# Performance work log

Measured on AMD Instinct MI355X. Metric: run time of the kernel, lower is better.

## Reference

```python
import jax, jax.numpy as jnp
import numpy as np

NUM_EMBEDDINGS = 8192
EMBEDDING_DIM = 32
L2_EPS = 1e-12  # matches torch F.normalize eps


def _l2_normalize(x, axis=-1):
    norm = jnp.linalg.norm(x, axis=axis, keepdims=True)
    return x / jnp.maximum(norm, L2_EPS)


def setup_inputs() -> dict:
    key = jax.random.key(0)
    k1, k2 = jax.random.split(key)
    inputs = jax.random.normal(k1, (32, 1024, EMBEDDING_DIM), dtype=jnp.float32)
    embeddings = jax.random.normal(k2, (NUM_EMBEDDINGS, EMBEDDING_DIM), dtype=jnp.float32)
    embeddings = _l2_normalize(embeddings, axis=1)  # buffer init: F.normalize(randn)
    return {"inputs": inputs, "embeddings": embeddings}


def reference(inputs, embeddings):
    input_shape = inputs.shape
    d = embeddings.shape[1]
    flat = inputs.reshape(-1, d)                      # [N, d]
    flat_n = _l2_normalize(flat, axis=1)              # F.normalize(flat, p=2, dim=1)
    # cosine similarity against codebook: [N, K]
    distances = jnp.einsum('nd,kd->nk', flat_n, embeddings)
    encoding_indices = jnp.argmax(distances, axis=1)  # [N]
    quantized = embeddings[encoding_indices].reshape(input_shape)
    # use_commitment=False branch: mse(quantized, inputs.detach())
    loss = jnp.mean((quantized - jax.lax.stop_gradient(inputs)) ** 2)
    # straight-through estimator
    quantized_st = inputs + jax.lax.stop_gradient(quantized - inputs)
    return quantized_st, loss, encoding_indices.reshape(input_shape[:-1])
```

## Files before the change

### kernel.cpp

```cpp
#include <hip/hip_runtime.h>

typedef short short8 __attribute__((ext_vector_type(8)));
typedef float f32x4 __attribute__((ext_vector_type(4)));

#define NROWS 32768
#define DIM 32
#define KCODES 8192
#define FLAG_CAP 16384
#define EPS_REL (1.0f/4096.0f)

#define WS_EHI  0
#define WS_ELO  (512*1024)
#define WS_PART (1024*1024)
#define WS_CNT  (WS_PART + 4096)
#define WS_LIST (WS_CNT + 64)
#define WS_CORR (WS_LIST + FLAG_CAP*4)

__device__ __forceinline__ unsigned short bf16_rne(float v){
    unsigned int u = __float_as_uint(v);
    unsigned int r = (u + 0x7fffu + ((u >> 16) & 1u)) >> 16;
    return (unsigned short)r;
}
__device__ __forceinline__ float bf16_to_f(unsigned short h){
    return __uint_as_float(((unsigned int)h) << 16);
}
__device__ __forceinline__ float dot4(const float4& a, const float4& b){
    return fmaf(a.w, b.w, fmaf(a.z, b.z, fmaf(a.y, b.y, a.x * b.x)));
}

__global__ __launch_bounds__(256) void vq_prep(
    const float* __restrict__ emb,
    unsigned short* __restrict__ ehi, unsigned short* __restrict__ elo,
    int* __restrict__ cnt)
{
    int r = blockIdx.x * 256 + threadIdx.x;
    if (r == 0) cnt[0] = 0;
    const float* er = emb + (size_t)r * DIM;
    short8* dh = (short8*)(ehi + (size_t)r * DIM);
    short8* dl = (short8*)(elo + (size_t)r * DIM);
    #pragma unroll
    for (int i = 0; i < 4; i++){
        float4 v0 = *(const float4*)(er + i*8);
        float4 v1 = *(const float4*)(er + i*8 + 4);
        float f[8] = {v0.x, v0.y, v0.z, v0.w, v1.x, v1.y, v1.z, v1.w};
        short8 a, b;
        #pragma unroll
        for (int j = 0; j < 8; j++){
            unsigned short h = bf16_rne(f[j]);
            a[j] = (short)h;
            b[j] = (short)bf16_rne(f[j] - bf16_to_f(h));
        }
        dh[i] = a; dl[i] = b;
    }
}

#define PROC(bhv, blv, tcs)                                                      \
  {                                                                              \
    unsigned int tcv = (unsigned int)(tcs);                                      \
    _Pragma("unroll")                                                            \
    for (int rg = 0; rg < 4; ++rg){                                              \
      f32x4 acc = __builtin_amdgcn_mfma_f32_16x16x32_bf16(ahi[rg], bhv, cbias[rg], 0, 0, 0); \
      acc = __builtin_amdgcn_mfma_f32_16x16x32_bf16(ahi[rg], blv, acc, 0, 0, 0); \
      acc = __builtin_amdgcn_mfma_f32_16x16x32_bf16(alo[rg], bhv, acc, 0, 0, 0); \
      _Pragma("unroll")                                                          \
      for (int q = 0; q < 4; ++q){                                               \
        unsigned int u = (__float_as_uint(acc[q]) & maskv) | tcv;                \
        int rr = rg * 4 + q;                                                     \
        unsigned int nv2;                                                        \
        asm("v_med3_u32 %0, %1, %2, %3" : "=v"(nv2) : "v"(u), "v"(v1[rr]), "v"(v2[rr])); \
        v2[rr] = nv2;                                                            \
        v1[rr] = max(u, v1[rr]);                                                 \
      }                                                                          \
    }                                                                            \
  }

__global__ __launch_bounds__(512, 4) void vq_main_mfma(
    const float* __restrict__ inputs,
    const unsigned short* __restrict__ ehi,
    const unsigned short* __restrict__ elo,
    const float* __restrict__ emb,
    float* __restrict__ out_q, float* __restrict__ out_idx,
    float* __restrict__ part, int* __restrict__ cnt, int* __restrict__ list)
{
    const int L = threadIdx.x & 63;
    const int w = threadIdx.x >> 6;
    const int rowbase = blockIdx.x * 64;

    __shared__ float snorm[64];
    __shared__ unsigned int sv1[8][64];
    __shared__ unsigned int sv2[8][64];
    __shared__ int          scol[8][64];

    short8 ahi[4], alo[4];
    #pragma unroll
    for (int rg = 0; rg < 4; ++rg){
        const float* xr = inputs + (size_t)(rowbase + rg*16 + (L & 15)) * DIM + (L >> 4) * 8;
        float4 p0 = *(const float4*)xr;
        float4 p1 = *(const float4*)(xr + 4);
        float f[8] = {p0.x, p0.y, p0.z, p0.w, p1.x, p1.y, p1.z, p1.w};
        short8 h, l;
        #pragma unroll
        for (int i = 0; i < 8; i++){
            unsigned short hb = bf16_rne(f[i]);
            h[i] = (short)hb;
            l[i] = (short)bf16_rne(f[i] - bf16_to_f(hb));
        }
        ahi[rg] = h; alo[rg] = l;
        float s = dot4(p0, p0) + dot4(p1, p1);
        s += __shfl_xor(s, 16, 64);
        s += __shfl_xor(s, 32, 64);
        if (w == 0 && (L >> 4) == 0) snorm[rg*16 + L] = sqrtf(s);
    }
    __syncthreads();

    f32x4 cbias[4];
    #pragma unroll
    for (int rg = 0; rg < 4; ++rg){
        #pragma unroll
        for (int q = 0; q < 4; ++q)
            cbias[rg][q] = 2.0f * snorm[rg*16 + (L >> 4)*4 + q];
    }

    unsigned int maskv = 0xFFFFFFC0u;
    asm("" : "+v"(maskv));

    unsigned int v1[16], v2[16];
    #pragma unroll
    for (int r = 0; r < 16; r++){ v1[r] = 0u; v2[r] = 0u; }

    const int c0 = w * 1024;
    const unsigned short* ehp = ehi + (size_t)(c0 + (L & 15)) * DIM + (L >> 4) * 8;
    const unsigned short* elp = elo + (size_t)(c0 + (L & 15)) * DIM + (L >> 4) * 8;

    for (int t = 0; t < 64; t += 2){
        short8 b0h = *(const short8*)(ehp);
        short8 b0l = *(const short8*)(elp);
        short8 b1h = *(const short8*)(ehp + 512);
        short8 b1l = *(const short8*)(elp + 512);
        ehp += 1024; elp += 1024;
        PROC(b0h, b0l, 63 - t);
        PROC(b1h, b1l, 62 - t);
    }

    unsigned int p1[16];
    #pragma unroll
    for (int r = 0; r < 16; r++) p1[r] = v1[r];
    #pragma unroll
    for (int m = 1; m < 16; m <<= 1){
        #pragma unroll
        for (int r = 0; r < 16; r++){
            unsigned int ov1 = __shfl_xor(v1[r], m, 64);
            unsigned int ov2 = __shfl_xor(v2[r], m, 64);
            unsigned int mn = min(v1[r], ov1);
            v2[r] = max(max(v2[r], ov2), mn);
            v1[r] = max(v1[r], ov1);
        }
    }
    int colr[16];
    #pragma unroll
    for (int r = 0; r < 16; r++){
        unsigned long long bm = __ballot(p1[r] == v1[r]);
        unsigned int grp = (unsigned int)((bm >> ((L >> 4) << 4)) & 0xFFFFull);
        colr[r] = __ffs(grp) - 1;
    }

    if ((L & 15) == 0){
        #pragma unroll
        for (int rg = 0; rg < 4; ++rg){
            #pragma unroll
            for (int q = 0; q < 4; ++q){
                int row = rg*16 + (L >> 4)*4 + q;
                sv1[w][row] = v1[rg*4 + q];
                sv2[w][row] = v2[rg*4 + q];
                scol[w][row] = colr[rg*4 + q];
            }
        }
    }
    __syncthreads();

    if (threadIdx.x < 64){
        int r = threadIdx.x;
        unsigned int b1 = 0u, b2 = 0u; int bw = 0, bc = 0;
        #pragma unroll
        for (int s = 0; s < 8; ++s){
            unsigned int u1 = sv1[s][r];
            unsigned int u2 = sv2[s][r];
            unsigned int mn = min(b1, u1);
            b2 = max(max(b2, u2), mn);
            bool g = u1 > b1;
            if (g){ b1 = u1; bw = s; bc = scol[s][r]; }
        }
        int t = 63 - (int)(b1 & 63u);
        int k = bw*1024 + t*16 + bc;
        int row = rowbase + r;
        out_idx[row] = (float)k;

        const float4* ep = (const float4*)(emb + (size_t)k * DIM);
        const float4* xr = (const float4*)(inputs + (size_t)row * DIM);
        float4* oq = (float4*)(out_q + (size_t)row * DIM);
        float s = 0.f;
        #pragma unroll
        for (int i = 0; i < 8; i++){
            float4 q = ep[i], x = xr[i];
            oq[i] = q;
            float dx = q.x - x.x, dy = q.y - x.y, dz = q.z - x.z, dw = q.w - x.w;
            s += dx*dx + dy*dy + dz*dz + dw*dw;
        }

        float f1 = __uint_as_float(b1 & 0xFFFFFFC0u);
        float f2 = __uint_as_float(b2 & 0xFFFFFFC0u);
        if (f1 - f2 <= snorm[r] * EPS_REL){
            int pos = atomicAdd(cnt, 1);
            if (pos < FLAG_CAP) list[pos] = row;
        }

        #pragma unroll
        for (int off = 32; off; off >>= 1) s += __shfl_down(s, off, 64);
        if (r == 0) part[blockIdx.x] = s;
    }
}

__global__ __launch_bounds__(256) void vq_refine(
    const float* __restrict__ inputs, const float* __restrict__ emb,
    float* __restrict__ out_q, float* __restrict__ out_idx,
    const int* __restrict__ list, const int* __restrict__ cnt,
    float* __restrict__ corrd)
{
    int n = *cnt; if (n > FLAG_CAP) n = FLAG_CAP;
    __shared__ float sv[4]; __shared__ int si[4];
    __shared__ int sbi;
    for (int j = blockIdx.x; j < n; j += gridDim.x){
        int row = list[j];
        const float4* xr = (const float4*)(inputs + (size_t)row * DIM);
        float4 x0 = xr[0], x1 = xr[1], x2 = xr[2], x3 = xr[3];
        float4 x4 = xr[4], x5 = xr[5], x6 = xr[6], x7 = xr[7];
        float bv = -3.0e38f; int bi = 0x7fffffff;
        for (int c = threadIdx.x; c < KCODES; c += 256){
            const float4* ep = (const float4*)(emb + (size_t)c * DIM);
            float d = dot4(x0, ep[0]) + dot4(x1, ep[1]) + dot4(x2, ep[2]) + dot4(x3, ep[3])
                    + dot4(x4, ep[4]) + dot4(x5, ep[5]) + dot4(x6, ep[6]) + dot4(x7, ep[7]);
            if (d > bv || (d == bv && c < bi)){ bv = d; bi = c; }
        }
        #pragma unroll
        for (int off = 32; off; off >>= 1){
            float ov = __shfl_down(bv, off, 64);
            int   oi = __shfl_down(bi, off, 64);
            if (ov > bv || (ov == bv && oi < bi)){ bv = ov; bi = oi; }
        }
        if ((threadIdx.x & 63) == 0){ sv[threadIdx.x >> 6] = bv; si[threadIdx.x >> 6] = bi; }
        __syncthreads();
        if (threadIdx.x == 0){
            #pragma unroll
            for (int q = 1; q < 4; q++){
                if (sv[q] > bv || (sv[q] == bv && si[q] < bi)){ bv = sv[q]; bi = si[q]; }
            }
            sbi = bi;
        }
        __syncthreads();
        int knew = sbi;
        int kold = (int)out_idx[row];
        if (threadIdx.x < 32){
            float x  = inputs[(size_t)row * DIM + threadIdx.x];
            float en = emb[(size_t)knew * DIM + threadIdx.x];
            float eo = emb[(size_t)kold * DIM + threadIdx.x];
            float d  = (en - x)*(en - x) - (eo - x)*(eo - x);
            #pragma unroll
            for (int off = 16; off; off >>= 1) d += __shfl_down(d, off, 64);
            if (knew != kold) out_q[(size_t)row * DIM + threadIdx.x] = en;
            if (threadIdx.x == 0){
                corrd[j] = (knew != kold) ? d : 0.0f;
                if (knew != kold) out_idx[row] = (float)knew;
            }
        }
        __syncthreads();
    }
}

__global__ __launch_bounds__(256) void vq_loss(
    const float* __restrict__ part, const float* __restrict__ corrd,
    const int* __restrict__ cnt, float* __restrict__ out_loss)
{
    int n = *cnt; if (n > FLAG_CAP) n = FLAG_CAP;
    float s = 0.f;
    for (int i = threadIdx.x; i < 512; i += 256) s += part[i];
    for (int j = threadIdx.x; j < n; j += 256) s += corrd[j];
    #pragma unroll
    for (int off = 32; off; off >>= 1) s += __shfl_down(s, off, 64);
    __shared__ float sp[4];
    if ((threadIdx.x & 63) == 0) sp[threadIdx.x >> 6] = s;
    __syncthreads();
    if (threadIdx.x == 0)
        *out_loss = (sp[0] + sp[1] + sp[2] + sp[3]) * (1.0f / ((float)NROWS * (float)DIM));
}

extern "C" void kernel_launch(void* const* d_in, const int* in_sizes, int n_in,
                              void* d_out, int out_size, void* d_ws, size_t ws_size,
                              hipStream_t stream) {
    const float* inputs = (const float*)d_in[0];
    const float* emb    = (const float*)d_in[1];
    float* out      = (float*)d_out;
    float* out_q    = out;
    float* out_loss = out + (size_t)NROWS * DIM;
    float* out_idx  = out_loss + 1;

    char* ws = (char*)d_ws;
    unsigned short* ehi   = (unsigned short*)(ws + WS_EHI);
    unsigned short* elo   = (unsigned short*)(ws + WS_ELO);
    float*          part  = (float*)(ws + WS_PART);
    int*            cnt   = (int*)(ws + WS_CNT);
    int*            list  = (int*)(ws + WS_LIST);
    float*          corrd = (float*)(ws + WS_CORR);

    vq_prep     <<<dim3(KCODES/256), dim3(256), 0, stream>>>(emb, ehi, elo, cnt);
    vq_main_mfma<<<dim3(NROWS/64),   dim3(512), 0, stream>>>(inputs, ehi, elo, emb,
                                                             out_q, out_idx, part, cnt, list);
    vq_refine   <<<dim3(256),        dim3(256), 0, stream>>>(inputs, emb, out_q, out_idx,
                                                             list, cnt, corrd);
    vq_loss     <<<dim3(1),          dim3(256), 0, stream>>>(part, corrd, cnt, out_loss);
}
```

Baseline: 98.76 us.

## Halve rows per block, fuse loss into refine, widen prep parallelism

The main MFMA kernel now handles 32 rows per block instead of 64, giving 1024 blocks instead of 512, with launch bounds raised to 8 waves per SIMD. The aim is to spread work over more CUs and raise occupancy. The separate loss kernel is removed: the last refine block to finish, detected with an atomic ticket counter, sums the partials. The prep kernel splits each codebook row across 4 threads. The trade-off is that each codebook tile loaded from memory is reused across half as many rows, so codebook traffic per row doubles.

```diff
diff --git a/kernel.cpp b/kernel.cpp
--- a/kernel.cpp
+++ b/kernel.cpp
@@ -8,6 +8,7 @@
 #define KCODES 8192
 #define FLAG_CAP 16384
 #define EPS_REL (1.0f/4096.0f)
+#define NBLK 1024
 
 #define WS_EHI  0
 #define WS_ELO  (512*1024)
@@ -33,32 +34,30 @@
     unsigned short* __restrict__ ehi, unsigned short* __restrict__ elo,
     int* __restrict__ cnt)
 {
-    int r = blockIdx.x * 256 + threadIdx.x;
-    if (r == 0) cnt[0] = 0;
-    const float* er = emb + (size_t)r * DIM;
-    short8* dh = (short8*)(ehi + (size_t)r * DIM);
-    short8* dl = (short8*)(elo + (size_t)r * DIM);
-    #pragma unroll
-    for (int i = 0; i < 4; i++){
-        float4 v0 = *(const float4*)(er + i*8);
-        float4 v1 = *(const float4*)(er + i*8 + 4);
-        float f[8] = {v0.x, v0.y, v0.z, v0.w, v1.x, v1.y, v1.z, v1.w};
-        short8 a, b;
-        #pragma unroll
-        for (int j = 0; j < 8; j++){
-            unsigned short h = bf16_rne(f[j]);
-            a[j] = (short)h;
-            b[j] = (short)bf16_rne(f[j] - bf16_to_f(h));
-        }
-        dh[i] = a; dl[i] = b;
-    }
+    int tid = blockIdx.x * 256 + threadIdx.x;
+    if (tid < 2) cnt[tid] = 0;
+    int r  = tid >> 2;
+    int qt = tid & 3;
+    const float* er = emb + (size_t)r * DIM + qt * 8;
+    float4 v0 = *(const float4*)er;
+    float4 v1 = *(const float4*)(er + 4);
+    float f[8] = {v0.x, v0.y, v0.z, v0.w, v1.x, v1.y, v1.z, v1.w};
+    short8 a, b;
+    #pragma unroll
+    for (int j = 0; j < 8; j++){
+        unsigned short h = bf16_rne(f[j]);
+        a[j] = (short)h;
+        b[j] = (short)bf16_rne(f[j] - bf16_to_f(h));
+    }
+    *(short8*)(ehi + (size_t)r * DIM + qt * 8) = a;
+    *(short8*)(elo + (size_t)r * DIM + qt * 8) = b;
 }
 
 #define PROC(bhv, blv, tcs)                                                      \
   {                                                                              \
     unsigned int tcv = (unsigned int)(tcs);                                      \
     _Pragma("unroll")                                                            \
-    for (int rg = 0; rg < 4; ++rg){                                              \
+    for (int rg = 0; rg < 2; ++rg){                                              \
       f32x4 acc = __builtin_amdgcn_mfma_f32_16x16x32_bf16(ahi[rg], bhv, cbias[rg], 0, 0, 0); \
       acc = __builtin_amdgcn_mfma_f32_16x16x32_bf16(ahi[rg], blv, acc, 0, 0, 0); \
       acc = __builtin_amdgcn_mfma_f32_16x16x32_bf16(alo[rg], bhv, acc, 0, 0, 0); \
@@ -74,7 +73,7 @@
     }                                                                            \
   }
 
-__global__ __launch_bounds__(512, 4) void vq_main_mfma(
+__global__ __launch_bounds__(512, 8) void vq_main_mfma(
     const float* __restrict__ inputs,
     const unsigned short* __restrict__ ehi,
     const unsigned short* __restrict__ elo,
@@ -84,16 +83,16 @@
 {
     const int L = threadIdx.x & 63;
     const int w = threadIdx.x >> 6;
-    const int rowbase = blockIdx.x * 64;
-
-    __shared__ float snorm[64];
-    __shared__ unsigned int sv1[8][64];
-    __shared__ unsigned int sv2[8][64];
-    __shared__ int          scol[8][64];
-
-    short8 ahi[4], alo[4];
-    #pragma unroll
-    for (int rg = 0; rg < 4; ++rg){
+    const int rowbase = blockIdx.x * 32;
+
+    __shared__ float snorm[32];
+    __shared__ unsigned int sv1[8][32];
+    __shared__ unsigned int sv2[8][32];
+    __shared__ int          scol[8][32];
+
+    short8 ahi[2], alo[2];
+    #pragma unroll
+    for (int rg = 0; rg < 2; ++rg){
         const float* xr = inputs + (size_t)(rowbase + rg*16 + (L & 15)) * DIM + (L >> 4) * 8;
         float4 p0 = *(const float4*)xr;
         float4 p1 = *(const float4*)(xr + 4);
@@ -113,9 +112,9 @@
     }
     __syncthreads();
 
-    f32x4 cbias[4];
-    #pragma unroll
-    for (int rg = 0; rg < 4; ++rg){
+    f32x4 cbias[2];
+    #pragma unroll
+    for (int rg = 0; rg < 2; ++rg){
         #pragma unroll
         for (int q = 0; q < 4; ++q)
             cbias[rg][q] = 2.0f * snorm[rg*16 + (L >> 4)*4 + q];
@@ -124,9 +123,9 @@
     unsigned int maskv = 0xFFFFFFC0u;
     asm("" : "+v"(maskv));
 
-    unsigned int v1[16], v2[16];
-    #pragma unroll
-    for (int r = 0; r < 16; r++){ v1[r] = 0u; v2[r] = 0u; }
+    unsigned int v1[8], v2[8];
+    #pragma unroll
+    for (int r = 0; r < 8; r++){ v1[r] = 0u; v2[r] = 0u; }
 
     const int c0 = w * 1024;
     const unsigned short* ehp = ehi + (size_t)(c0 + (L & 15)) * DIM + (L >> 4) * 8;
@@ -142,13 +141,13 @@
         PROC(b1h, b1l, 62 - t);
     }
 
-    unsigned int p1[16];
-    #pragma unroll
-    for (int r = 0; r < 16; r++) p1[r] = v1[r];
+    unsigned int p1[8];
+    #pragma unroll
+    for (int r = 0; r < 8; r++) p1[r] = v1[r];
     #pragma unroll
     for (int m = 1; m < 16; m <<= 1){
         #pragma unroll
-        for (int r = 0; r < 16; r++){
+        for (int r = 0; r < 8; r++){
             unsigned int ov1 = __shfl_xor(v1[r], m, 64);
             unsigned int ov2 = __shfl_xor(v2[r], m, 64);
             unsigned int mn = min(v1[r], ov1);
@@ -156,9 +155,9 @@
             v1[r] = max(v1[r], ov1);
         }
     }
-    int colr[16];
-    #pragma unroll
-    for (int r = 0; r < 16; r++){
+    int colr[8];
+    #pragma unroll
+    for (int r = 0; r < 8; r++){
         unsigned long long bm = __ballot(p1[r] == v1[r]);
         unsigned int grp = (unsigned int)((bm >> ((L >> 4) << 4)) & 0xFFFFull);
         colr[r] = __ffs(grp) - 1;
@@ -166,7 +165,7 @@
 
     if ((L & 15) == 0){
         #pragma unroll
-        for (int rg = 0; rg < 4; ++rg){
+        for (int rg = 0; rg < 2; ++rg){
             #pragma unroll
             for (int q = 0; q < 4; ++q){
                 int row = rg*16 + (L >> 4)*4 + q;
@@ -178,7 +177,7 @@
     }
     __syncthreads();
 
-    if (threadIdx.x < 64){
+    if (threadIdx.x < 32){
         int r = threadIdx.x;
         unsigned int b1 = 0u, b2 = 0u; int bw = 0, bc = 0;
         #pragma unroll
@@ -215,7 +214,7 @@
         }
 
         #pragma unroll
-        for (int off = 32; off; off >>= 1) s += __shfl_down(s, off, 64);
+        for (int off = 16; off; off >>= 1) s += __shfl_down(s, off, 64);
         if (r == 0) part[blockIdx.x] = s;
     }
 }
@@ -223,10 +222,11 @@
 __global__ __launch_bounds__(256) void vq_refine(
     const float* __restrict__ inputs, const float* __restrict__ emb,
     float* __restrict__ out_q, float* __restrict__ out_idx,
-    const int* __restrict__ list, const int* __restrict__ cnt,
-    float* __restrict__ corrd)
+    const int* __restrict__ list, int* __restrict__ cnt,
+    float* __restrict__ corrd, const float* __restrict__ part,
+    float* __restrict__ out_loss)
 {
-    int n = *cnt; if (n > FLAG_CAP) n = FLAG_CAP;
+    int n = cnt[0]; if (n > FLAG_CAP) n = FLAG_CAP;
     __shared__ float sv[4]; __shared__ int si[4];
     __shared__ int sbi;
     for (int j = blockIdx.x; j < n; j += gridDim.x){
@@ -274,23 +274,26 @@
         }
         __syncthreads();
     }
-}
-
-__global__ __launch_bounds__(256) void vq_loss(
-    const float* __restrict__ part, const float* __restrict__ corrd,
-    const int* __restrict__ cnt, float* __restrict__ out_loss)
-{
-    int n = *cnt; if (n > FLAG_CAP) n = FLAG_CAP;
-    float s = 0.f;
-    for (int i = threadIdx.x; i < 512; i += 256) s += part[i];
-    for (int j = threadIdx.x; j < n; j += 256) s += corrd[j];
-    #pragma unroll
-    for (int off = 32; off; off >>= 1) s += __shfl_down(s, off, 64);
-    __shared__ float sp[4];
-    if ((threadIdx.x & 63) == 0) sp[threadIdx.x >> 6] = s;
+
+    __shared__ int tkt;
+    if (threadIdx.x == 0){
+        __threadfence();
+        tkt = atomicAdd(cnt + 1, 1);
+    }
     __syncthreads();
-    if (threadIdx.x == 0)
-        *out_loss = (sp[0] + sp[1] + sp[2] + sp[3]) * (1.0f / ((float)NROWS * (float)DIM));
+    if (tkt == (int)gridDim.x - 1){
+        __threadfence();
+        float s = 0.f;
+        for (int i = threadIdx.x; i < NBLK; i += 256) s += part[i];
+        for (int j = threadIdx.x; j < n; j += 256) s += corrd[j];
+        #pragma unroll
+        for (int off = 32; off; off >>= 1) s += __shfl_down(s, off, 64);
+        __shared__ float sp[4];
+        if ((threadIdx.x & 63) == 0) sp[threadIdx.x >> 6] = s;
+        __syncthreads();
+        if (threadIdx.x == 0)
+            *out_loss = (sp[0] + sp[1] + sp[2] + sp[3]) * (1.0f / ((float)NROWS * (float)DIM));
+    }
 }
 
 extern "C" void kernel_launch(void* const* d_in, const int* in_sizes, int n_in,
@@ -311,10 +314,9 @@
     int*            list  = (int*)(ws + WS_LIST);
     float*          corrd = (float*)(ws + WS_CORR);
 
-    vq_prep     <<<dim3(KCODES/256), dim3(256), 0, stream>>>(emb, ehi, elo, cnt);
-    vq_main_mfma<<<dim3(NROWS/64),   dim3(512), 0, stream>>>(inputs, ehi, elo, emb,
-                                                             out_q, out_idx, part, cnt, list);
-    vq_refine   <<<dim3(256),        dim3(256), 0, stream>>>(inputs, emb, out_q, out_idx,
-                                                             list, cnt, corrd);
-    vq_loss     <<<dim3(1),          dim3(256), 0, stream>>>(part, corrd, cnt, out_loss);
-}
+    vq_prep     <<<dim3(128),  dim3(256), 0, stream>>>(emb, ehi, elo, cnt);
+    vq_main_mfma<<<dim3(NBLK), dim3(512), 0, stream>>>(inputs, ehi, elo, emb,
+                                                       out_q, out_idx, part, cnt, list);
+    vq_refine   <<<dim3(256),  dim3(256), 0, stream>>>(inputs, emb, out_q, out_idx,
+                                                       list, cnt, corrd, part, out_loss);
+}
```

New measurement: 219.1 us. +121.9%, slower.

## Fuse refine and loss into main kernel with last-block ticket reduction

Applied to the files above, without the earlier changes.

Moves exact fp32 refinement of ambiguous rows into the main MFMA kernel, with each block handling its own flagged rows through a shared-memory list. The final loss reduction is done by the last block to finish, found with an atomic ticket, which removes two kernel launches and the global flag list. The change also software-prefetches codebook fragments one iteration ahead and gives the prep kernel four threads per code row for more parallelism. The cost is that each block's refinement now runs serially inside that block, and blocks with many flagged rows could become stragglers.

```diff
diff --git a/kernel.cpp b/kernel.cpp
--- a/kernel.cpp
+++ b/kernel.cpp
@@ -6,15 +6,13 @@
 #define NROWS 32768
 #define DIM 32
 #define KCODES 8192
-#define FLAG_CAP 16384
 #define EPS_REL (1.0f/4096.0f)
+#define NBLK 512
 
 #define WS_EHI  0
 #define WS_ELO  (512*1024)
 #define WS_PART (1024*1024)
 #define WS_CNT  (WS_PART + 4096)
-#define WS_LIST (WS_CNT + 64)
-#define WS_CORR (WS_LIST + FLAG_CAP*4)
 
 __device__ __forceinline__ unsigned short bf16_rne(float v){
     unsigned int u = __float_as_uint(v);
@@ -33,25 +31,23 @@
     unsigned short* __restrict__ ehi, unsigned short* __restrict__ elo,
     int* __restrict__ cnt)
 {
-    int r = blockIdx.x * 256 + threadIdx.x;
-    if (r == 0) cnt[0] = 0;
-    const float* er = emb + (size_t)r * DIM;
-    short8* dh = (short8*)(ehi + (size_t)r * DIM);
-    short8* dl = (short8*)(elo + (size_t)r * DIM);
-    #pragma unroll
-    for (int i = 0; i < 4; i++){
-        float4 v0 = *(const float4*)(er + i*8);
-        float4 v1 = *(const float4*)(er + i*8 + 4);
-        float f[8] = {v0.x, v0.y, v0.z, v0.w, v1.x, v1.y, v1.z, v1.w};
-        short8 a, b;
-        #pragma unroll
-        for (int j = 0; j < 8; j++){
-            unsigned short h = bf16_rne(f[j]);
-            a[j] = (short)h;
-            b[j] = (short)bf16_rne(f[j] - bf16_to_f(h));
-        }
-        dh[i] = a; dl[i] = b;
-    }
+    int tid = blockIdx.x * 256 + threadIdx.x;
+    if (tid < 2) cnt[tid] = 0;
+    int r  = tid >> 2;
+    int qt = tid & 3;
+    const float* er = emb + (size_t)r * DIM + qt * 8;
+    float4 v0 = *(const float4*)er;
+    float4 v1 = *(const float4*)(er + 4);
+    float f[8] = {v0.x, v0.y, v0.z, v0.w, v1.x, v1.y, v1.z, v1.w};
+    short8 a, b;
+    #pragma unroll
+    for (int j = 0; j < 8; j++){
+        unsigned short h = bf16_rne(f[j]);
+        a[j] = (short)h;
+        b[j] = (short)bf16_rne(f[j] - bf16_to_f(h));
+    }
+    *(short8*)(ehi + (size_t)r * DIM + qt * 8) = a;
+    *(short8*)(elo + (size_t)r * DIM + qt * 8) = b;
 }
 
 #define PROC(bhv, blv, tcs)                                                      \
@@ -80,7 +76,7 @@
     const unsigned short* __restrict__ elo,
     const float* __restrict__ emb,
     float* __restrict__ out_q, float* __restrict__ out_idx,
-    float* __restrict__ part, int* __restrict__ cnt, int* __restrict__ list)
+    float* __restrict__ part, int* __restrict__ ticket, float* __restrict__ out_loss)
 {
     const int L = threadIdx.x & 63;
     const int w = threadIdx.x >> 6;
@@ -90,6 +86,15 @@
     __shared__ unsigned int sv1[8][64];
     __shared__ unsigned int sv2[8][64];
     __shared__ int          scol[8][64];
+    __shared__ float s_loss[64];
+    __shared__ int   s_k[64];
+    __shared__ int   sflag[64];
+    __shared__ int   snf, s_newk;
+    __shared__ float swv[8];
+    __shared__ int   swi[8];
+    __shared__ int   tkt;
+
+    if (threadIdx.x == 0) snf = 0;
 
     short8 ahi[4], alo[4];
     #pragma unroll
@@ -132,15 +137,22 @@
     const unsigned short* ehp = ehi + (size_t)(c0 + (L & 15)) * DIM + (L >> 4) * 8;
     const unsigned short* elp = elo + (size_t)(c0 + (L & 15)) * DIM + (L >> 4) * 8;
 
-    for (int t = 0; t < 64; t += 2){
-        short8 b0h = *(const short8*)(ehp);
-        short8 b0l = *(const short8*)(elp);
-        short8 b1h = *(const short8*)(ehp + 512);
-        short8 b1l = *(const short8*)(elp + 512);
+    short8 nb0h = *(const short8*)(ehp);
+    short8 nb0l = *(const short8*)(elp);
+    short8 nb1h = *(const short8*)(ehp + 512);
+    short8 nb1l = *(const short8*)(elp + 512);
+    for (int t = 0; t < 62; t += 2){
+        short8 b0h = nb0h, b0l = nb0l, b1h = nb1h, b1l = nb1l;
         ehp += 1024; elp += 1024;
+        nb0h = *(const short8*)(ehp);
+        nb0l = *(const short8*)(elp);
+        nb1h = *(const short8*)(ehp + 512);
+        nb1l = *(const short8*)(elp + 512);
         PROC(b0h, b0l, 63 - t);
         PROC(b1h, b1l, 62 - t);
     }
+    PROC(nb0h, nb0l, 1);
+    PROC(nb1h, nb1l, 0);
 
     unsigned int p1[16];
     #pragma unroll
@@ -194,6 +206,7 @@
         int k = bw*1024 + t*16 + bc;
         int row = rowbase + r;
         out_idx[row] = (float)k;
+        s_k[r] = k;
 
         const float4* ep = (const float4*)(emb + (size_t)k * DIM);
         const float4* xr = (const float4*)(inputs + (size_t)row * DIM);
@@ -206,36 +219,26 @@
             float dx = q.x - x.x, dy = q.y - x.y, dz = q.z - x.z, dw = q.w - x.w;
             s += dx*dx + dy*dy + dz*dz + dw*dw;
         }
+        s_loss[r] = s;
 
         float f1 = __uint_as_float(b1 & 0xFFFFFFC0u);
         float f2 = __uint_as_float(b2 & 0xFFFFFFC0u);
         if (f1 - f2 <= snorm[r] * EPS_REL){
-            int pos = atomicAdd(cnt, 1);
-            if (pos < FLAG_CAP) list[pos] = row;
-        }
-
-        #pragma unroll
-        for (int off = 32; off; off >>= 1) s += __shfl_down(s, off, 64);
-        if (r == 0) part[blockIdx.x] = s;
-    }
-}
-
-__global__ __launch_bounds__(256) void vq_refine(
-    const float* __restrict__ inputs, const float* __restrict__ emb,
-    float* __restrict__ out_q, float* __restrict__ out_idx,
-    const int* __restrict__ list, const int* __restrict__ cnt,
-    float* __restrict__ corrd)
-{
-    int n = *cnt; if (n > FLAG_CAP) n = FLAG_CAP;
-    __shared__ float sv[4]; __shared__ int si[4];
-    __shared__ int sbi;
-    for (int j = blockIdx.x; j < n; j += gridDim.x){
-        int row = list[j];
+            int pos = atomicAdd(&snf, 1);
+            sflag[pos] = r;
+        }
+    }
+    __syncthreads();
+
+    int nf = snf;
+    for (int j = 0; j < nf; ++j){
+        int r = sflag[j];
+        int row = rowbase + r;
         const float4* xr = (const float4*)(inputs + (size_t)row * DIM);
         float4 x0 = xr[0], x1 = xr[1], x2 = xr[2], x3 = xr[3];
         float4 x4 = xr[4], x5 = xr[5], x6 = xr[6], x7 = xr[7];
         float bv = -3.0e38f; int bi = 0x7fffffff;
-        for (int c = threadIdx.x; c < KCODES; c += 256){
+        for (int c = threadIdx.x; c < KCODES; c += 512){
             const float4* ep = (const float4*)(emb + (size_t)c * DIM);
             float d = dot4(x0, ep[0]) + dot4(x1, ep[1]) + dot4(x2, ep[2]) + dot4(x3, ep[3])
                     + dot4(x4, ep[4]) + dot4(x5, ep[5]) + dot4(x6, ep[6]) + dot4(x7, ep[7]);
@@ -247,50 +250,58 @@
             int   oi = __shfl_down(bi, off, 64);
             if (ov > bv || (ov == bv && oi < bi)){ bv = ov; bi = oi; }
         }
-        if ((threadIdx.x & 63) == 0){ sv[threadIdx.x >> 6] = bv; si[threadIdx.x >> 6] = bi; }
+        if (L == 0){ swv[w] = bv; swi[w] = bi; }
         __syncthreads();
         if (threadIdx.x == 0){
             #pragma unroll
-            for (int q = 1; q < 4; q++){
-                if (sv[q] > bv || (sv[q] == bv && si[q] < bi)){ bv = sv[q]; bi = si[q]; }
+            for (int q = 1; q < 8; q++){
+                if (swv[q] > bv || (swv[q] == bv && swi[q] < bi)){ bv = swv[q]; bi = swi[q]; }
             }
-            sbi = bi;
+            s_newk = bi;
         }
         __syncthreads();
-        int knew = sbi;
-        int kold = (int)out_idx[row];
-        if (threadIdx.x < 32){
-            float x  = inputs[(size_t)row * DIM + threadIdx.x];
-            float en = emb[(size_t)knew * DIM + threadIdx.x];
-            float eo = emb[(size_t)kold * DIM + threadIdx.x];
-            float d  = (en - x)*(en - x) - (eo - x)*(eo - x);
+        int knew = s_newk;
+        if (knew != s_k[r]){
+            if (threadIdx.x < 32){
+                float x  = inputs[(size_t)row * DIM + threadIdx.x];
+                float en = emb[(size_t)knew * DIM + threadIdx.x];
+                out_q[(size_t)row * DIM + threadIdx.x] = en;
+                float d = (en - x) * (en - x);
+                #pragma unroll
+                for (int off = 16; off; off >>= 1) d += __shfl_down(d, off, 32);
+                if (threadIdx.x == 0){ s_loss[r] = d; out_idx[row] = (float)knew; }
+            }
+        }
+        __syncthreads();
+    }
+
+    if (threadIdx.x < 64){
+        float s = s_loss[threadIdx.x];
+        #pragma unroll
+        for (int off = 32; off; off >>= 1) s += __shfl_down(s, off, 64);
+        if (threadIdx.x == 0) part[blockIdx.x] = s;
+    }
+
+    if (threadIdx.x == 0){
+        __threadfence();
+        tkt = atomicAdd(ticket, 1);
+    }
+    __syncthreads();
+    if (tkt == NBLK - 1){
+        __threadfence();
+        float s = part[threadIdx.x];
+        #pragma unroll
+        for (int off = 32; off; off >>= 1) s += __shfl_down(s, off, 64);
+        __shared__ float sp[8];
+        if (L == 0) sp[w] = s;
+        __syncthreads();
+        if (threadIdx.x == 0){
+            float tot = 0.f;
             #pragma unroll
-            for (int off = 16; off; off >>= 1) d += __shfl_down(d, off, 64);
-            if (knew != kold) out_q[(size_t)row * DIM + threadIdx.x] = en;
-            if (threadIdx.x == 0){
-                corrd[j] = (knew != kold) ? d : 0.0f;
-                if (knew != kold) out_idx[row] = (float)knew;
-            }
-        }
-        __syncthreads();
-    }
-}
-
-__global__ __launch_bounds__(256) void vq_loss(
-    const float* __restrict__ part, const float* __restrict__ corrd,
-    const int* __restrict__ cnt, float* __restrict__ out_loss)
-{
-    int n = *cnt; if (n > FLAG_CAP) n = FLAG_CAP;
-    float s = 0.f;
-    for (int i = threadIdx.x; i < 512; i += 256) s += part[i];
-    for (int j = threadIdx.x; j < n; j += 256) s += corrd[j];
-    #pragma unroll
-    for (int off = 32; off; off >>= 1) s += __shfl_down(s, off, 64);
-    __shared__ float sp[4];
-    if ((threadIdx.x & 63) == 0) sp[threadIdx.x >> 6] = s;
-    __syncthreads();
-    if (threadIdx.x == 0)
-        *out_loss = (sp[0] + sp[1] + sp[2] + sp[3]) * (1.0f / ((float)NROWS * (float)DIM));
+            for (int q = 0; q < 8; q++) tot += sp[q];
+            *out_loss = tot * (1.0f / ((float)NROWS * (float)DIM));
+        }
+    }
 }
 
 extern "C" void kernel_launch(void* const* d_in, const int* in_sizes, int n_in,
@@ -304,17 +315,12 @@
     float* out_idx  = out_loss + 1;
 
     char* ws = (char*)d_ws;
-    unsigned short* ehi   = (unsigned short*)(ws + WS_EHI);
-    unsigned short* elo   = (unsigned short*)(ws + WS_ELO);
-    float*          part  = (float*)(ws + WS_PART);
-    int*            cnt   = (int*)(ws + WS_CNT);
-    int*            list  = (int*)(ws + WS_LIST);
-    float*          corrd = (float*)(ws + WS_CORR);
-
-    vq_prep     <<<dim3(KCODES/256), dim3(256), 0, stream>>>(emb, ehi, elo, cnt);
-    vq_main_mfma<<<dim3(NROWS/64),   dim3(512), 0, stream>>>(inputs, ehi, elo, emb,
-                                                             out_q, out_idx, part, cnt, list);
-    vq_refine   <<<dim3(256),        dim3(256), 0, stream>>>(inputs, emb, out_q, out_idx,
-                                                             list, cnt, corrd);
-    vq_loss     <<<dim3(1),          dim3(256), 0, stream>>>(part, corrd, cnt, out_loss);
-}
+    unsigned short* ehi  = (unsigned short*)(ws + WS_EHI);
+    unsigned short* elo  = (unsigned short*)(ws + WS_ELO);
+    float*          part = (float*)(ws + WS_PART);
+    int*            cnt  = (int*)(ws + WS_CNT);
+
+    vq_prep     <<<dim3(128),  dim3(256), 0, stream>>>(emb, ehi, elo, cnt);
+    vq_main_mfma<<<dim3(NBLK), dim3(512), 0, stream>>>(inputs, ehi, elo, emb,
+                                                       out_q, out_idx, part, cnt + 1, out_loss);
+}
```

Measured after the change: 210.6 us. 113% more time.
